# Kernel optimization log

Hardware: AMD Instinct MI355X
Metric: run time of the kernel (lower is better)

Reference implementation:

```python
import jax, jax.numpy as jnp
import numpy as np

BATCH = 16384
XD = 64      # x_dim
AD = 16      # a_dim
NC = 8       # number of constraints
PEN = 10.0   # relax_penalty
DELTA = 1.0  # class-K coefficient
ITERS = 250  # FISTA iterations for the dual QP (converges to OSQP solution)


def _cbf_forward(a_des, x, A, B, Qc, cc, dc):
    """Batched CBF-QP safety filter.

    Constraints: g_i(x) = 0.5 x^T Qc_i x + cc_i^T x - dc_i  (g_i <= 0 is safe)
    Barrier:     h_i(x) = -g_i(x),  grad_h = -(Qc_i x + cc_i)
    QP:  min ||a - a_des||^2 + PEN * ||s||^2
         s.t. Lg_h a >= -Lf_h - DELTA*h - s,  s >= 0
    Solved exactly (to FISTA tolerance) via the dual:
         min_{lam>=0} 0.5 lam^T M lam - lam^T q,
    with z = [a; s], H = diag(2*1_AD, 2*PEN*1_NC), z = z0 + H^{-1} G^T lam.
    """
    bsz = a_des.shape[0]
    # constraint values and gradients (the 'autograd jacobian' in the original)
    g_x = 0.5 * jnp.einsum('bi,mij,bj->bm', x, Qc, x) + x @ cc.T - dc[None, :]
    h_x = -g_x                                              # [B, NC]
    grad_h = -(jnp.einsum('mij,bj->bmi', Qc, x) + cc[None])  # [B, NC, XD]
    # Lie derivatives
    Lf_h = jnp.einsum('bmi,bij,bj->bm', grad_h, A, x)        # [B, NC]
    Lg_h = jnp.einsum('bmi,bia->bma', grad_h, B)             # [B, NC, AD]
    bvec = -Lf_h - DELTA * h_x                               # rhs: Lg_h a + s >= bvec

    # dual QP setup: G z >= c, G = [[Lg_h, I],[0, I]], c = [bvec; 0]
    Im = jnp.broadcast_to(jnp.eye(NC, dtype=a_des.dtype), (bsz, NC, NC))
    Gtop = jnp.concatenate([Lg_h, Im], axis=2)                    # [B, NC, AD+NC]
    Gbot = jnp.concatenate([jnp.zeros((bsz, NC, AD), a_des.dtype), Im], axis=2)
    G = jnp.concatenate([Gtop, Gbot], axis=1)                     # [B, 2NC, AD+NC]
    dinv = jnp.concatenate([0.5 * jnp.ones(AD, a_des.dtype),
                            jnp.ones(NC, a_des.dtype) / (2.0 * PEN)])
    Mmat = jnp.einsum('bkn,n,bln->bkl', G, dinv, G)               # [B, 2NC, 2NC]
    q = jnp.concatenate([bvec - jnp.einsum('bma,ba->bm', Lg_h, a_des),
                         jnp.zeros((bsz, NC), a_des.dtype)], axis=1)

    # step size 1/L, L = max eigenvalue of M (not differentiated)
    L = jax.lax.stop_gradient(jnp.linalg.eigvalsh(Mmat)[..., -1]) + 1e-6
    t = (1.0 / L)[:, None]

    lam0 = jnp.zeros((bsz, 2 * NC), a_des.dtype)

    def step(carry, _):
        lam, y, tk = carry
        grad = jnp.einsum('bkl,bl->bk', Mmat, y) - q
        lam_new = jnp.maximum(y - t * grad, 0.0)
        tk1 = 0.5 * (1.0 + jnp.sqrt(1.0 + 4.0 * tk * tk))
        y_new = lam_new + ((tk - 1.0) / tk1) * (lam_new - lam)
        return (lam_new, y_new, tk1), None

    (lam, _, _), _ = jax.lax.scan(step, (lam0, lam0, jnp.float32(1.0)), None, length=ITERS)

    # primal recovery: a = a_des + 0.5 * Lg_h^T lam_top
    a_safe = a_des + 0.5 * jnp.einsum('bma,bm->ba', Lg_h, lam[:, :NC])
    return a_safe


def setup_inputs() -> dict:
    key = jax.random.key(0)
    ks = jax.random.split(key, 7)
    a_des = jax.random.normal(ks[0], (BATCH, AD), jnp.float32)
    x = jax.random.normal(ks[1], (BATCH, XD), jnp.float32)
    A = jax.random.normal(ks[2], (BATCH, XD, XD), jnp.float32) * 0.05
    B = jax.random.normal(ks[3], (BATCH, XD, AD), jnp.float32) * 0.1
    R = jax.random.normal(ks[4], (NC, XD, XD), jnp.float32) * 0.05
    Qc = R + jnp.swapaxes(R, 1, 2)  # symmetric quadratic constraint Hessians
    cc = jax.random.normal(ks[5], (NC, XD), jnp.float32) * 0.1
    dc = jax.random.uniform(ks[6], (NC,), jnp.float32) + 0.5
    return {"a_des": a_des, "x": x, "A": A, "B": B, "Qc": Qc, "cc": cc, "dc": dc}


def reference(a_des, x, A, B, Qc, cc, dc):
    return _cbf_forward(a_des, x, A, B, Qc, cc, dc)
```

## Files before the change

### kernel.cpp

```cpp
#include <hip/hip_runtime.h>
#include <cstddef>

#define NBATCH 16384

struct Betas {
  float b[250];
  static constexpr double csqrt(double x) {
    double g = x > 1.0 ? x : 1.0;
    for (int i = 0; i < 64; ++i) g = 0.5 * (g + x / g);
    return g;
  }
  constexpr Betas() : b{} {
    double tk = 1.0;
    for (int i = 0; i < 250; ++i) {
      double tk1 = 0.5 * (1.0 + csqrt(1.0 + 4.0 * tk * tk));
      b[i] = (float)((tk - 1.0) / tk1);
      tk = tk1;
    }
  }
};
__device__ constexpr Betas BETAS{};

template <int CTRL>
__device__ __forceinline__ float fdpp(float v) {
  return __int_as_float(
      __builtin_amdgcn_mov_dpp(__float_as_int(v), CTRL, 0xF, 0xF, true));
}
__device__ __forceinline__ float rowsum16(float p) {
  p += fdpp<0x121>(p);
  p += fdpp<0x122>(p);
  p += fdpp<0x124>(p);
  p += fdpp<0x128>(p);
  return p;
}

__global__ __launch_bounds__(256) void cbf_k1_gh(
    const float* __restrict__ Qc, const float* __restrict__ cc,
    const float* __restrict__ X, float* __restrict__ gh) {
  __shared__ float xt[128 * 65];
  __shared__ float qt[128 * 65];
  __shared__ float cct[128];
  const int tid = threadIdx.x;
  const int b0 = (blockIdx.x >> 2) * 128;
  const int r0 = (blockIdx.x & 3) * 128;

#pragma unroll
  for (int i = 0; i < 8; ++i) {
    const int g   = i * 256 + tid;
    const int row = g >> 4;
    const int c4  = g & 15;
    float4 v = *(const float4*)(X  + (size_t)(b0 + row) * 64 + c4 * 4);
    float4 w = *(const float4*)(Qc + (size_t)(r0 + row) * 64 + c4 * 4);
    *(float4*)&xt[row * 65 + c4 * 4] = v;
    *(float4*)&qt[row * 65 + c4 * 4] = w;
  }
  if (tid < 128) cct[tid] = cc[r0 + tid];
  __syncthreads();

  const int w  = tid >> 6;
  const int bw = (w & 1) * 64;
  const int rw = (w >> 1) * 64;
  const int bi = (tid & 7) * 8;
  const int rj = ((tid >> 3) & 7) * 8;
  const float* xb = xt + (bw + bi) * 65;
  const float* qb = qt + (rw + rj) * 65;

  float acc[8][8] = {};
#pragma unroll 2
  for (int cg = 0; cg < 16; ++cg) {
    float4 xa[8], qa[8];
#pragma unroll
    for (int i = 0; i < 8; ++i) xa[i] = *(const float4*)&xb[i * 65 + cg * 4];
#pragma unroll
    for (int j = 0; j < 8; ++j) qa[j] = *(const float4*)&qb[j * 65 + cg * 4];
#pragma unroll
    for (int i = 0; i < 8; ++i)
#pragma unroll
      for (int j = 0; j < 8; ++j) {
        acc[i][j] = fmaf(xa[i].x, qa[j].x, acc[i][j]);
        acc[i][j] = fmaf(xa[i].y, qa[j].y, acc[i][j]);
        acc[i][j] = fmaf(xa[i].z, qa[j].z, acc[i][j]);
        acc[i][j] = fmaf(xa[i].w, qa[j].w, acc[i][j]);
      }
  }

  float cc8[8];
  *(float4*)&cc8[0] = *(const float4*)&cct[rw + rj];
  *(float4*)&cc8[4] = *(const float4*)&cct[rw + rj + 4];
  const int gr = r0 + rw + rj;
#pragma unroll
  for (int i = 0; i < 8; ++i) {
    float o[8];
#pragma unroll
    for (int j = 0; j < 8; ++j) o[j] = acc[i][j] + cc8[j];
    float* dst = gh + (size_t)(b0 + bw + bi + i) * 512 + gr;
    *(float4*)dst       = *(const float4*)&o[0];
    *(float4*)(dst + 4) = *(const float4*)&o[4];
  }
}

#define XOFF  0
#define BVOFF 64
#define BOFF  72
#define GHOFF (72 + 1024)
#define LGOFF (1096 + 544)
#define AXOFF (1640 + 160)
#define ESTR  (1800 + 64)

__global__ __launch_bounds__(256) void cbf_k2_setup(
    const float* __restrict__ X, const float* __restrict__ Abat,
    const float* __restrict__ Bbat, const float* __restrict__ cc,
    const float* __restrict__ dc, const float* __restrict__ a_des,
    const float* __restrict__ gh, float* __restrict__ S_ws,
    float* __restrict__ LgT_ws, float* __restrict__ qu_ws) {
  __shared__ float smem[4 * ESTR];
  const int tid  = threadIdx.x;
  const int sub  = tid >> 6;
  const int lane = tid & 63;
  const int b    = blockIdx.x * 4 + sub;
  float* sm = smem + sub * ESTR;

  const float xi = X[(size_t)b * 64 + lane];
  sm[XOFF + lane] = xi;
  {
    const float4* bp = (const float4*)(Bbat + (size_t)b * 1024);
#pragma unroll
    for (int n = 0; n < 4; ++n) {
      float4 v = bp[n * 64 + lane];
      *(float4*)&sm[BOFF + n * 256 + lane * 4] = v;
    }
  }
  {
    const float4* gp = (const float4*)(gh + (size_t)b * 512);
    float4 g0 = gp[lane];
    float4 g1 = gp[64 + lane];
    const int f0 = lane * 4, f1 = 256 + lane * 4;
    *(float4*)&sm[GHOFF + (f0 >> 6) * 68 + (f0 & 63)] = g0;
    *(float4*)&sm[GHOFF + (f1 >> 6) * 68 + (f1 & 63)] = g1;
  }
  __syncthreads();

  {
    const float4* ap = (const float4*)(Abat + (size_t)b * 4096);
    const int cg = lane & 15;
    const int rg = lane >> 4;
    const float4 xv = *(const float4*)&sm[XOFF + cg * 4];
#pragma unroll
    for (int n = 0; n < 16; ++n) {
      float4 av = ap[n * 64 + lane];
      float p = av.x * xv.x + av.y * xv.y + av.z * xv.z + av.w * xv.w;
      p = rowsum16(p);
      if (cg == 0) sm[AXOFF + n * 4 + rg] = p;
    }
  }
  __syncthreads();

  {
    const int m  = lane >> 3;
    const int ig = lane & 7;
    const float4 ghA = *(const float4*)&sm[GHOFF + m * 68 + ig * 8];
    const float4 ghB = *(const float4*)&sm[GHOFF + m * 68 + ig * 8 + 4];
    const float4 xA  = *(const float4*)&sm[XOFF + ig * 8];
    const float4 xB  = *(const float4*)&sm[XOFF + ig * 8 + 4];
    const float4 axA = *(const float4*)&sm[AXOFF + ig * 8];
    const float4 axB = *(const float4*)&sm[AXOFF + ig * 8 + 4];
    const float4 ccA = *(const float4*)(cc + m * 64 + ig * 8);
    const float4 ccB = *(const float4*)(cc + m * 64 + ig * 8 + 4);
    float p1 = ghA.x * xA.x + ghA.y * xA.y + ghA.z * xA.z + ghA.w * xA.w
             + ghB.x * xB.x + ghB.y * xB.y + ghB.z * xB.z + ghB.w * xB.w;
    float p2 = ghA.x * axA.x + ghA.y * axA.y + ghA.z * axA.z + ghA.w * axA.w
             + ghB.x * axB.x + ghB.y * axB.y + ghB.z * axB.z + ghB.w * axB.w;
    float p3 = ccA.x * xA.x + ccA.y * xA.y + ccA.z * xA.z + ccA.w * xA.w
             + ccB.x * xB.x + ccB.y * xB.y + ccB.z * xB.z + ccB.w * xB.w;
    p1 += __shfl_xor(p1, 1); p1 += __shfl_xor(p1, 2); p1 += __shfl_xor(p1, 4);
    p2 += __shfl_xor(p2, 1); p2 += __shfl_xor(p2, 2); p2 += __shfl_xor(p2, 4);
    p3 += __shfl_xor(p3, 1); p3 += __shfl_xor(p3, 2); p3 += __shfl_xor(p3, 4);
    if (ig == 0) {
      sm[BVOFF + m] = p2 + 0.5f * (p1 + p3) - dc[m];
    }
  }

  const int mq  = lane >> 3;
  const int ap2 = lane & 7;
  {
    float acc0 = 0.f, acc1 = 0.f;
#pragma unroll
    for (int c = 0; c < 16; ++c) {
      float4 gv = *(const float4*)&sm[GHOFF + mq * 68 + 4 * c];
#pragma unroll
      for (int n = 0; n < 4; ++n) {
        float2 bv2 = *(const float2*)&sm[BOFF + (4 * c + n) * 16 + 2 * ap2];
        float gvn = (n == 0) ? gv.x : ((n == 1) ? gv.y : ((n == 2) ? gv.z : gv.w));
        acc0 = fmaf(gvn, bv2.x, acc0);
        acc1 = fmaf(gvn, bv2.y, acc1);
      }
    }
    const float lg0 = -acc0, lg1 = -acc1;
    LgT_ws[(size_t)b * 128 + (2 * ap2) * 8 + mq]     = lg0;
    LgT_ws[(size_t)b * 128 + (2 * ap2 + 1) * 8 + mq] = lg1;
    sm[LGOFF + mq * 20 + 2 * ap2]     = lg0;
    sm[LGOFF + mq * 20 + 2 * ap2 + 1] = lg1;
  }
  __syncthreads();

  const int kq = lane >> 3;
  const int lq = lane & 7;
  {
    float s = 0.f;
#pragma unroll
    for (int c = 0; c < 4; ++c) {
      float4 ka = *(const float4*)&sm[LGOFF + kq * 20 + 4 * c];
      float4 la = *(const float4*)&sm[LGOFF + lq * 20 + 4 * c];
      s = fmaf(ka.x, la.x, s);
      s = fmaf(ka.y, la.y, s);
      s = fmaf(ka.z, la.z, s);
      s = fmaf(ka.w, la.w, s);
    }
    S_ws[(size_t)b * 64 + kq * 8 + lq] = 0.5f * s;
  }

  {
    float2 ad2 = *(const float2*)(a_des + (size_t)b * 16 + 2 * lq);
    float2 kg  = *(const float2*)&sm[LGOFF + kq * 20 + 2 * lq];
    float p = kg.x * ad2.x + kg.y * ad2.y;
    p += __shfl_xor(p, 1);
    p += __shfl_xor(p, 2);
    p += __shfl_xor(p, 4);
    if (lq == 0) qu_ws[(size_t)b * 8 + kq] = sm[BVOFF + kq] - p;
  }
}

__global__ __launch_bounds__(256) void cbf_k3_fista(
    const float* __restrict__ S_ws, const float* __restrict__ qu_ws,
    const float* __restrict__ LgT_ws, const float* __restrict__ a_des,
    float* __restrict__ out) {
  const int gt = blockIdx.x * 256 + threadIdx.x;
  const int e  = gt >> 2;
  const int q  = gt & 3;

  const float4* Sp = (const float4*)(S_ws + (size_t)e * 64);
  const float4 sl0 = Sp[q * 2],       sl1 = Sp[q * 2 + 1];
  const float4 sh0 = Sp[(q + 4) * 2], sh1 = Sp[(q + 4) * 2 + 1];
  const float qu_lo = qu_ws[(size_t)e * 8 + q];
  const float qu_hi = qu_ws[(size_t)e * 8 + q + 4];

#define MV(ylo, yhi, alo, ahi) do {                                          \
    float b0 = fdpp<0x00>(ylo), b1 = fdpp<0x55>(ylo);                        \
    float b2 = fdpp<0xAA>(ylo), b3 = fdpp<0xFF>(ylo);                        \
    float b4 = fdpp<0x00>(yhi), b5 = fdpp<0x55>(yhi);                        \
    float b6 = fdpp<0xAA>(yhi), b7 = fdpp<0xFF>(yhi);                        \
    float t0 = sl0.x * b0, t1 = sl0.y * b1;                                  \
    t0 = fmaf(sl0.z, b2, t0); t1 = fmaf(sl0.w, b3, t1);                      \
    t0 = fmaf(sl1.x, b4, t0); t1 = fmaf(sl1.y, b5, t1);                      \
    t0 = fmaf(sl1.z, b6, t0); t1 = fmaf(sl1.w, b7, t1);                      \
    alo = t0 + t1;                                                           \
    float u0 = sh0.x * b0, u1 = sh0.y * b1;                                  \
    u0 = fmaf(sh0.z, b2, u0); u1 = fmaf(sh0.w, b3, u1);                      \
    u0 = fmaf(sh1.x, b4, u0); u1 = fmaf(sh1.y, b5, u1);                      \
    u0 = fmaf(sh1.z, b6, u0); u1 = fmaf(sh1.w, b7, u1);                      \
    ahi = u0 + u1;                                                           \
  } while (0)

  float vl = 1.f, vh = 1.f, svl, svh;
#pragma unroll 4
  for (int it = 0; it < 40; ++it) {
    MV(vl, vh, svl, svh);
    float am = fmaxf(fabsf(svl), fabsf(svh));
    am = fmaxf(am, fdpp<0xB1>(am));
    am = fmaxf(am, fdpp<0x4E>(am));
    float r = 1.f / fmaxf(am, 1e-30f);
    vl = svl * r; vh = svh * r;
  }
  MV(vl, vh, svl, svh);
  float num = vl * svl + vh * svh;
  float den = vl * vl + vh * vh;
  num += fdpp<0xB1>(num); den += fdpp<0xB1>(den);
  num += fdpp<0x4E>(num); den += fdpp<0x4E>(den);
  float mu = fmaxf((num / fmaxf(den, 1e-30f)) * 1.001f, 0.f);
  const float lmax = 0.5f * ((0.1f + mu) + sqrtf(fmaf(mu, mu, 0.01f)));
  const float t = 1.0f / (lmax + 1e-6f);

  float yul = 0.f, yuh = 0.f, yvl = 0.f, yvh = 0.f;
  float lul = 0.f, luh = 0.f, lvl_ = 0.f, lvh = 0.f;
#pragma unroll 5
  for (int it = 0; it < 250; ++it) {
    const float beta = BETAS.b[it];
    const float wl = 0.05f * (yul + yvl);
    const float wh = 0.05f * (yuh + yvh);
    float al, ah;
    MV(yul, yuh, al, ah);
    const float gul = al + wl - qu_lo;
    const float guh = ah + wh - qu_hi;
    const float lunl = fmaxf(fmaf(-t, gul, yul), 0.f);
    const float lunh = fmaxf(fmaf(-t, guh, yuh), 0.f);
    const float lvnl = fmaxf(fmaf(-t, wl, yvl), 0.f);
    const float lvnh = fmaxf(fmaf(-t, wh, yvh), 0.f);
    yul = fmaf(beta, lunl - lul, lunl); lul = lunl;
    yuh = fmaf(beta, lunh - luh, lunh); luh = lunh;
    yvl = fmaf(beta, lvnl - lvl_, lvnl); lvl_ = lvnl;
    yvh = fmaf(beta, lvnh - lvh, lvnh); lvh = lvnh;
  }
#undef MV

  const float l0 = fdpp<0x00>(lul), l1 = fdpp<0x55>(lul);
  const float l2 = fdpp<0xAA>(lul), l3 = fdpp<0xFF>(lul);
  const float l4 = fdpp<0x00>(luh), l5 = fdpp<0x55>(luh);
  const float l6 = fdpp<0xAA>(luh), l7 = fdpp<0xFF>(luh);
  const float4* Lp = (const float4*)(LgT_ws + (size_t)e * 128 + q * 32);
  const float4 ad  = *(const float4*)(a_des + (size_t)e * 16 + q * 4);
  float o[4];
#pragma unroll
  for (int j = 0; j < 4; ++j) {
    float4 ga = Lp[j * 2], gb = Lp[j * 2 + 1];
    float s = ga.x * l0 + ga.y * l1 + ga.z * l2 + ga.w * l3
            + gb.x * l4 + gb.y * l5 + gb.z * l6 + gb.w * l7;
    o[j] = 0.5f * s;
  }
  float4 ov;
  ov.x = ad.x + o[0]; ov.y = ad.y + o[1];
  ov.z = ad.z + o[2]; ov.w = ad.w + o[3];
  *(float4*)(out + (size_t)e * 16 + q * 4) = ov;
}

extern "C" void kernel_launch(void* const* d_in, const int* in_sizes, int n_in,
                              void* d_out, int out_size, void* d_ws, size_t ws_size,
                              hipStream_t stream) {
  (void)in_sizes; (void)n_in; (void)out_size; (void)ws_size;
  const float* a_des = (const float*)d_in[0];
  const float* x     = (const float*)d_in[1];
  const float* A     = (const float*)d_in[2];
  const float* B     = (const float*)d_in[3];
  const float* Qc    = (const float*)d_in[4];
  const float* cc    = (const float*)d_in[5];
  const float* dc    = (const float*)d_in[6];
  float* out = (float*)d_out;

  float* gh  = (float*)d_ws;
  float* S   = gh  + (size_t)NBATCH * 512;
  float* LgT = S   + (size_t)NBATCH * 64;
  float* qu  = LgT + (size_t)NBATCH * 128;

  hipLaunchKernelGGL(cbf_k1_gh, dim3(512), dim3(256), 0, stream, Qc, cc, x, gh);
  hipLaunchKernelGGL(cbf_k2_setup, dim3(4096), dim3(256), 0, stream,
                     x, A, B, cc, dc, a_des, gh, S, LgT, qu);
  hipLaunchKernelGGL(cbf_k3_fista, dim3(256), dim3(256), 0, stream,
                     S, qu, LgT, a_des, out);
}
```

Measured before the change: 488.8 us.

## Fuse setup and FISTA kernels so the dual QP solve reads from shared memory

Merges the setup kernel and the FISTA solver kernel into one. Each 64-lane sub-block now runs the power iteration and the 250 FISTA steps with four of its lanes, taking S, q and Lg_h straight from shared memory. This removes one launch and the global workspace writes and reads of S, LgT and q. In exchange, only 4 of 64 lanes do useful work during the long serial FISTA loop, so that loop issues about 16 times more wave instructions. Its speed then depends on many waves per SIMD hiding latency.

```diff
diff --git a/kernel.cpp b/kernel.cpp
--- a/kernel.cpp
+++ b/kernel.cpp
@@ -107,12 +107,11 @@
 #define AXOFF (1640 + 160)
 #define ESTR  (1800 + 64)
 
-__global__ __launch_bounds__(256) void cbf_k2_setup(
+__global__ __launch_bounds__(256) void cbf_k23(
     const float* __restrict__ X, const float* __restrict__ Abat,
     const float* __restrict__ Bbat, const float* __restrict__ cc,
     const float* __restrict__ dc, const float* __restrict__ a_des,
-    const float* __restrict__ gh, float* __restrict__ S_ws,
-    float* __restrict__ LgT_ws, float* __restrict__ qu_ws) {
+    const float* __restrict__ gh, float* __restrict__ out) {
   __shared__ float smem[4 * ESTR];
   const int tid  = threadIdx.x;
   const int sub  = tid >> 6;
@@ -195,11 +194,8 @@
         acc1 = fmaf(gvn, bv2.y, acc1);
       }
     }
-    const float lg0 = -acc0, lg1 = -acc1;
-    LgT_ws[(size_t)b * 128 + (2 * ap2) * 8 + mq]     = lg0;
-    LgT_ws[(size_t)b * 128 + (2 * ap2 + 1) * 8 + mq] = lg1;
-    sm[LGOFF + mq * 20 + 2 * ap2]     = lg0;
-    sm[LGOFF + mq * 20 + 2 * ap2 + 1] = lg1;
+    sm[LGOFF + mq * 20 + 2 * ap2]     = -acc0;
+    sm[LGOFF + mq * 20 + 2 * ap2 + 1] = -acc1;
   }
   __syncthreads();
 
@@ -216,7 +212,7 @@
       s = fmaf(ka.z, la.z, s);
       s = fmaf(ka.w, la.w, s);
     }
-    S_ws[(size_t)b * 64 + kq * 8 + lq] = 0.5f * s;
+    sm[AXOFF + kq * 8 + lq] = 0.5f * s;
   }
 
   {
@@ -226,23 +222,17 @@
     p += __shfl_xor(p, 1);
     p += __shfl_xor(p, 2);
     p += __shfl_xor(p, 4);
-    if (lq == 0) qu_ws[(size_t)b * 8 + kq] = sm[BVOFF + kq] - p;
-  }
-}
-
-__global__ __launch_bounds__(256) void cbf_k3_fista(
-    const float* __restrict__ S_ws, const float* __restrict__ qu_ws,
-    const float* __restrict__ LgT_ws, const float* __restrict__ a_des,
-    float* __restrict__ out) {
-  const int gt = blockIdx.x * 256 + threadIdx.x;
-  const int e  = gt >> 2;
-  const int q  = gt & 3;
-
-  const float4* Sp = (const float4*)(S_ws + (size_t)e * 64);
-  const float4 sl0 = Sp[q * 2],       sl1 = Sp[q * 2 + 1];
-  const float4 sh0 = Sp[(q + 4) * 2], sh1 = Sp[(q + 4) * 2 + 1];
-  const float qu_lo = qu_ws[(size_t)e * 8 + q];
-  const float qu_hi = qu_ws[(size_t)e * 8 + q + 4];
+    if (lq == 0) sm[BVOFF + kq] = sm[BVOFF + kq] - p;
+  }
+
+  if (lane < 4) {
+    const int q = lane;
+    const float4 sl0 = *(const float4*)&sm[AXOFF + q * 8];
+    const float4 sl1 = *(const float4*)&sm[AXOFF + q * 8 + 4];
+    const float4 sh0 = *(const float4*)&sm[AXOFF + (q + 4) * 8];
+    const float4 sh1 = *(const float4*)&sm[AXOFF + (q + 4) * 8 + 4];
+    const float qu_lo = sm[BVOFF + q];
+    const float qu_hi = sm[BVOFF + q + 4];
 
 #define MV(ylo, yhi, alo, ahi) do {                                          \
     float b0 = fdpp<0x00>(ylo), b1 = fdpp<0x55>(ylo);                        \
@@ -261,65 +251,67 @@
     ahi = u0 + u1;                                                           \
   } while (0)
 
-  float vl = 1.f, vh = 1.f, svl, svh;
+    float vl = 1.f, vh = 1.f, svl, svh;
 #pragma unroll 4
-  for (int it = 0; it < 40; ++it) {
+    for (int it = 0; it < 40; ++it) {
+      MV(vl, vh, svl, svh);
+      float am = fmaxf(fabsf(svl), fabsf(svh));
+      am = fmaxf(am, fdpp<0xB1>(am));
+      am = fmaxf(am, fdpp<0x4E>(am));
+      float r = 1.f / fmaxf(am, 1e-30f);
+      vl = svl * r; vh = svh * r;
+    }
     MV(vl, vh, svl, svh);
-    float am = fmaxf(fabsf(svl), fabsf(svh));
-    am = fmaxf(am, fdpp<0xB1>(am));
-    am = fmaxf(am, fdpp<0x4E>(am));
-    float r = 1.f / fmaxf(am, 1e-30f);
-    vl = svl * r; vh = svh * r;
-  }
-  MV(vl, vh, svl, svh);
-  float num = vl * svl + vh * svh;
-  float den = vl * vl + vh * vh;
-  num += fdpp<0xB1>(num); den += fdpp<0xB1>(den);
-  num += fdpp<0x4E>(num); den += fdpp<0x4E>(den);
-  float mu = fmaxf((num / fmaxf(den, 1e-30f)) * 1.001f, 0.f);
-  const float lmax = 0.5f * ((0.1f + mu) + sqrtf(fmaf(mu, mu, 0.01f)));
-  const float t = 1.0f / (lmax + 1e-6f);
-
-  float yul = 0.f, yuh = 0.f, yvl = 0.f, yvh = 0.f;
-  float lul = 0.f, luh = 0.f, lvl_ = 0.f, lvh = 0.f;
+    float num = vl * svl + vh * svh;
+    float den = vl * vl + vh * vh;
+    num += fdpp<0xB1>(num); den += fdpp<0xB1>(den);
+    num += fdpp<0x4E>(num); den += fdpp<0x4E>(den);
+    float mu = fmaxf((num / fmaxf(den, 1e-30f)) * 1.001f, 0.f);
+    const float lmax = 0.5f * ((0.1f + mu) + sqrtf(fmaf(mu, mu, 0.01f)));
+    const float t = 1.0f / (lmax + 1e-6f);
+
+    float yul = 0.f, yuh = 0.f, yvl = 0.f, yvh = 0.f;
+    float lul = 0.f, luh = 0.f, lvl_ = 0.f, lvh = 0.f;
 #pragma unroll 5
-  for (int it = 0; it < 250; ++it) {
-    const float beta = BETAS.b[it];
-    const float wl = 0.05f * (yul + yvl);
-    const float wh = 0.05f * (yuh + yvh);
-    float al, ah;
-    MV(yul, yuh, al, ah);
-    const float gul = al + wl - qu_lo;
-    const float guh = ah + wh - qu_hi;
-    const float lunl = fmaxf(fmaf(-t, gul, yul), 0.f);
-    const float lunh = fmaxf(fmaf(-t, guh, yuh), 0.f);
-    const float lvnl = fmaxf(fmaf(-t, wl, yvl), 0.f);
-    const float lvnh = fmaxf(fmaf(-t, wh, yvh), 0.f);
-    yul = fmaf(beta, lunl - lul, lunl); lul = lunl;
-    yuh = fmaf(beta, lunh - luh, lunh); luh = lunh;
-    yvl = fmaf(beta, lvnl - lvl_, lvnl); lvl_ = lvnl;
-    yvh = fmaf(beta, lvnh - lvh, lvnh); lvh = lvnh;
-  }
+    for (int it = 0; it < 250; ++it) {
+      const float beta = BETAS.b[it];
+      const float wl = 0.05f * (yul + yvl);
+      const float wh = 0.05f * (yuh + yvh);
+      float al, ah;
+      MV(yul, yuh, al, ah);
+      const float gul = al + wl - qu_lo;
+      const float guh = ah + wh - qu_hi;
+      const float lunl = fmaxf(fmaf(-t, gul, yul), 0.f);
+      const float lunh = fmaxf(fmaf(-t, guh, yuh), 0.f);
+      const float lvnl = fmaxf(fmaf(-t, wl, yvl), 0.f);
+      const float lvnh = fmaxf(fmaf(-t, wh, yvh), 0.f);
+      yul = fmaf(beta, lunl - lul, lunl); lul = lunl;
+      yuh = fmaf(beta, lunh - luh, lunh); luh = lunh;
+      yvl = fmaf(beta, lvnl - lvl_, lvnl); lvl_ = lvnl;
+      yvh = fmaf(beta, lvnh - lvh, lvnh); lvh = lvnh;
+    }
 #undef MV
 
-  const float l0 = fdpp<0x00>(lul), l1 = fdpp<0x55>(lul);
-  const float l2 = fdpp<0xAA>(lul), l3 = fdpp<0xFF>(lul);
-  const float l4 = fdpp<0x00>(luh), l5 = fdpp<0x55>(luh);
-  const float l6 = fdpp<0xAA>(luh), l7 = fdpp<0xFF>(luh);
-  const float4* Lp = (const float4*)(LgT_ws + (size_t)e * 128 + q * 32);
-  const float4 ad  = *(const float4*)(a_des + (size_t)e * 16 + q * 4);
-  float o[4];
-#pragma unroll
-  for (int j = 0; j < 4; ++j) {
-    float4 ga = Lp[j * 2], gb = Lp[j * 2 + 1];
-    float s = ga.x * l0 + ga.y * l1 + ga.z * l2 + ga.w * l3
-            + gb.x * l4 + gb.y * l5 + gb.z * l6 + gb.w * l7;
-    o[j] = 0.5f * s;
-  }
-  float4 ov;
-  ov.x = ad.x + o[0]; ov.y = ad.y + o[1];
-  ov.z = ad.z + o[2]; ov.w = ad.w + o[3];
-  *(float4*)(out + (size_t)e * 16 + q * 4) = ov;
+    const float l0 = fdpp<0x00>(lul), l1 = fdpp<0x55>(lul);
+    const float l2 = fdpp<0xAA>(lul), l3 = fdpp<0xFF>(lul);
+    const float l4 = fdpp<0x00>(luh), l5 = fdpp<0x55>(luh);
+    const float l6 = fdpp<0xAA>(luh), l7 = fdpp<0xFF>(luh);
+    const float4 ad = *(const float4*)(a_des + (size_t)b * 16 + q * 4);
+    float o[4];
+#pragma unroll
+    for (int j = 0; j < 4; ++j) {
+      const int a = q * 4 + j;
+      float s = sm[LGOFF + 0 * 20 + a] * l0 + sm[LGOFF + 1 * 20 + a] * l1
+              + sm[LGOFF + 2 * 20 + a] * l2 + sm[LGOFF + 3 * 20 + a] * l3
+              + sm[LGOFF + 4 * 20 + a] * l4 + sm[LGOFF + 5 * 20 + a] * l5
+              + sm[LGOFF + 6 * 20 + a] * l6 + sm[LGOFF + 7 * 20 + a] * l7;
+      o[j] = 0.5f * s;
+    }
+    float4 ov;
+    ov.x = ad.x + o[0]; ov.y = ad.y + o[1];
+    ov.z = ad.z + o[2]; ov.w = ad.w + o[3];
+    *(float4*)(out + (size_t)b * 16 + q * 4) = ov;
+  }
 }
 
 extern "C" void kernel_launch(void* const* d_in, const int* in_sizes, int n_in,
@@ -335,14 +327,9 @@
   const float* dc    = (const float*)d_in[6];
   float* out = (float*)d_out;
 
-  float* gh  = (float*)d_ws;
-  float* S   = gh  + (size_t)NBATCH * 512;
-  float* LgT = S   + (size_t)NBATCH * 64;
-  float* qu  = LgT + (size_t)NBATCH * 128;
+  float* gh = (float*)d_ws;
 
   hipLaunchKernelGGL(cbf_k1_gh, dim3(512), dim3(256), 0, stream, Qc, cc, x, gh);
-  hipLaunchKernelGGL(cbf_k2_setup, dim3(4096), dim3(256), 0, stream,
-                     x, A, B, cc, dc, a_des, gh, S, LgT, qu);
-  hipLaunchKernelGGL(cbf_k3_fista, dim3(256), dim3(256), 0, stream,
-                     S, qu, LgT, a_des, out);
-}
+  hipLaunchKernelGGL(cbf_k23, dim3(4096), dim3(256), 0, stream,
+                     x, A, B, cc, dc, a_des, gh, out);
+}
```

Measured after the change: 718.8 us. 1.47x slower.
